# Kernel optimization log

Hardware: AMD Instinct MI355X
Metric: run time of the kernel (lower is better)

## Reference

```python
import jax, jax.numpy as jnp
import numpy as np

B, V_IN, V_OUT, C_IN, C_OUT, K, NNZ = 16, 1024, 4096, 128, 256, 18, 16384

def setup_inputs() -> dict:
    key = jax.random.key(0)
    ks = jax.random.split(key, 10)
    def lin(k, fan_in, fan_out):
        s = 1.0 / np.sqrt(fan_in)
        return jax.random.normal(k, (fan_in, fan_out), jnp.float32) * s
    return {
        "x": jax.random.normal(ks[0], (B, V_IN, C_IN), jnp.float32),
        "vals": jax.random.uniform(ks[1], (NNZ,), jnp.float32),
        "W1": lin(ks[2], 1 * C_IN, C_OUT),
        "b1": jnp.zeros((C_OUT,), jnp.float32),
        "Wd3": lin(ks[3], (K // 3) * C_IN, C_OUT // 4),
        "bd3": jnp.zeros((C_OUT // 4,), jnp.float32),
        "W2d3": lin(ks[4], (K // 3 * 2) * C_IN, C_OUT // 4),
        "b2d3": jnp.zeros((C_OUT // 4,), jnp.float32),
        "Wf": lin(ks[5], K * C_IN, C_OUT // 2),
        "bf": jnp.zeros((C_OUT // 2,), jnp.float32),
        "rows": jax.random.randint(ks[6], (NNZ,), 0, V_OUT, jnp.int32),
        "cols": jax.random.randint(ks[7], (NNZ,), 0, V_IN, jnp.int32),
        "spiral_idx": jax.random.randint(ks[8], (V_OUT, K), 0, V_OUT, jnp.int32),
    }

def _pool(x, rows, cols, vals, dim_size):
    # sparse upsample: gather cols, scale, scatter-add to rows
    gathered = x[:, cols, :] * vals[None, :, None]  # [B, nnz, C]
    return jnp.zeros((x.shape[0], dim_size, x.shape[2]), x.dtype).at[:, rows, :].add(gathered)

def _spiral_conv(feat, idx, W, b):
    # gather fixed spiral neighborhoods then shared linear layer
    Bz, V, C = feat.shape[0], idx.shape[0], feat.shape[2]
    g = feat[:, idx.reshape(-1), :].reshape(Bz, V, idx.shape[1] * C)  # [B, V, K*C]
    return g @ W + b

def reference(x, vals, W1, b1, Wd3, bd3, W2d3, b2d3, Wf, bf, rows, cols, spiral_idx):
    out = _pool(x, rows, cols, vals, V_OUT)  # [B, V_OUT, C_IN]
    k = spiral_idx.shape[1]
    short_cut = _spiral_conv(out, spiral_idx[:, :1], W1, b1)
    p_d3 = _spiral_conv(out, spiral_idx[:, : k // 3], Wd3, bd3)
    p_2d3 = _spiral_conv(out, spiral_idx[:, : k // 3 * 2], W2d3, b2d3)
    p = _spiral_conv(out, spiral_idx, Wf, bf)
    f = jnp.concatenate((p, p_2d3, p_d3), axis=2)  # [B, V_OUT, C_OUT]
    return jax.nn.relu(short_cut + f)
```

## Files before the change

### kernel.cpp

```cpp
#include <hip/hip_runtime.h>
#include <hip/hip_bf16.h>

#define B_SZ   16
#define V_IN   1024
#define V_OUT  4096
#define C_IN   128
#define C_OUT  256
#define K_NB   18
#define NNZ    16384
#define K_GEMM (K_NB * C_IN)
#define BK     64
#define NKT    (K_GEMM / BK)

typedef __attribute__((ext_vector_type(8))) short bf16x8;
typedef __attribute__((ext_vector_type(4))) float f32x4;

#define GLOAD16(src, dst) __builtin_amdgcn_global_load_lds( \
    (const __attribute__((address_space(1))) unsigned int*)(src), \
    (__attribute__((address_space(3))) unsigned int*)(dst), 16, 0, 0)

#define MFMA16(a_, b_, c_) __builtin_amdgcn_mfma_f32_16x16x32_bf16((a_), (b_), (c_), 0, 0, 0)

__global__ void hist_kernel(const int* __restrict__ rows, int* counts) {
    int n = blockIdx.x * blockDim.x + threadIdx.x;
    if (n < NNZ) atomicAdd(&counts[rows[n]], 1);
}

__global__ void scan_kernel(const int* __restrict__ counts, int* offsets, int* cursor) {
    __shared__ int wsum[16];
    int t = threadIdx.x;
    int lane = t & 63, wid = t >> 6;
    int base4 = t * 4;
    int c0 = counts[base4], c1 = counts[base4 + 1], c2 = counts[base4 + 2], c3 = counts[base4 + 3];
    int tot = c0 + c1 + c2 + c3;
    int v = tot;
#pragma unroll
    for (int d = 1; d < 64; d <<= 1) {
        int u = __shfl_up(v, d);
        if (lane >= d) v += u;
    }
    if (lane == 63) wsum[wid] = v;
    __syncthreads();
    int wbase = 0;
#pragma unroll
    for (int w = 0; w < 16; ++w) wbase += (w < wid) ? wsum[w] : 0;
    int incl = wbase + v;
    int excl = incl - tot;
    offsets[base4]     = excl;
    offsets[base4 + 1] = excl + c0;
    offsets[base4 + 2] = excl + c0 + c1;
    offsets[base4 + 3] = excl + c0 + c1 + c2;
    cursor[base4]     = excl;
    cursor[base4 + 1] = excl + c0;
    cursor[base4 + 2] = excl + c0 + c1;
    cursor[base4 + 3] = excl + c0 + c1 + c2;
    if (t == 1023) offsets[V_OUT] = incl;
}

__global__ void fill_kernel(const int* __restrict__ rows, int* cursor, int* perm) {
    int n = blockIdx.x * blockDim.x + threadIdx.x;
    if (n < NNZ) {
        int r = rows[n];
        int pos = atomicAdd(&cursor[r], 1);
        perm[pos] = n;
    }
}

__global__ __launch_bounds__(512) void pool_kernel(
    const float* __restrict__ x, const float* __restrict__ vals,
    const int* __restrict__ cols, const int* __restrict__ offsets,
    const int* __restrict__ perm, __hip_bfloat16* __restrict__ pool) {
    int r = blockIdx.x;
    int t = threadIdx.x;
    int b = t >> 5, c4 = t & 31;
    int j0 = offsets[r], j1 = offsets[r + 1];
    const float4* xb = (const float4*)x + (size_t)b * (V_IN * 32);
    float4 acc = {0.f, 0.f, 0.f, 0.f};
    for (int j = j0; j < j1; ++j) {
        int n = perm[j];
        float v = vals[n];
        float4 xv = xb[cols[n] * 32 + c4];
        acc.x += v * xv.x; acc.y += v * xv.y; acc.z += v * xv.z; acc.w += v * xv.w;
    }
    ushort4 o;
    o.x = __builtin_bit_cast(unsigned short, __float2bfloat16(acc.x));
    o.y = __builtin_bit_cast(unsigned short, __float2bfloat16(acc.y));
    o.z = __builtin_bit_cast(unsigned short, __float2bfloat16(acc.z));
    o.w = __builtin_bit_cast(unsigned short, __float2bfloat16(acc.w));
    ((ushort4*)pool)[((size_t)b * V_OUT + r) * 32 + c4] = o;
}

__global__ void wcomb_kernel(const float* __restrict__ W1, const float* __restrict__ Wd3,
                             const float* __restrict__ W2d3, const float* __restrict__ Wf,
                             const float* __restrict__ b1, const float* __restrict__ bd3,
                             const float* __restrict__ b2d3, const float* __restrict__ bf,
                             __hip_bfloat16* __restrict__ wTs, float* __restrict__ bias) {
    int idx = blockIdx.x * blockDim.x + threadIdx.x;
    if (idx >= NKT * 16384) {
        int c = idx - NKT * 16384;
        if (c < C_OUT) {
            float v = b1[c];
            if (c < 128)      v += bf[c];
            else if (c < 192) v += b2d3[c - 128];
            else              v += bd3[c - 192];
            bias[c] = v;
        }
        return;
    }
    int kt = idx >> 14;
    int c  = (idx >> 3) & 2047;
    int e  = idx & 7;
    int nrow  = c >> 3;
    int kslot = (c & 7) << 4;
    int kb = kslot ^ ((nrow & 7) << 4);
    int r  = kt * 64 + (kb >> 1) + e;
    int col = nrow;
    float v;
    if (col < 128)      v = Wf[r * 128 + col];
    else if (col < 192) v = (r < 1536) ? W2d3[r * 64 + (col - 128)] : 0.f;
    else                v = (r < 768)  ? Wd3[r * 64 + (col - 192)]  : 0.f;
    if (r < 128) v += W1[r * 256 + col];
    wTs[idx] = __float2bfloat16(v);
}

__global__ __launch_bounds__(512, 2) void gemm_kernel(
    const __hip_bfloat16* __restrict__ pool,
    const __hip_bfloat16* __restrict__ wTs,
    const float* __restrict__ bias,
    const int* __restrict__ spiral,
    float* __restrict__ out)
{
    __shared__ __align__(16) char smem[116736];
    int* spl = (int*)(smem + 98304);

    const int tid  = threadIdx.x;
    const int lane = tid & 63;
    const int wid  = tid >> 6;
    const int q    = wid & 3;
    const int wm   = (wid >> 2) << 7;

    const int bid = blockIdx.x;
    const int bm  = ((bid & 7) << 5) + (bid >> 3);
    const int b   = bm >> 4;
    const int v0  = (bm & 15) << 8;

    for (int i = tid; i < 256 * K_NB; i += 512) spl[i] = spiral[v0 * K_NB + i];
    asm volatile("s_waitcnt vmcnt(0) lgkmcnt(0)" ::: "memory");
    __builtin_amdgcn_s_barrier();

    const char* poolBytes = (const char*)(pool + (size_t)b * V_OUT * C_IN);
    const char* wTsBytes  = (const char*)wTs;
    const int sb = ((tid & 7) << 4) ^ (((tid >> 3) & 7) << 4);

    auto stageA = [&](int kt, int slot) {
        const int j   = kt >> 1;
        const int c0b = (kt & 1) << 7;
        char* dst = smem + (slot << 15);
#pragma unroll
        for (int ch = 0; ch < 4; ++ch) {
            int row  = (ch << 6) + (tid >> 3);
            int sidx = spl[row * K_NB + j];
            GLOAD16(poolBytes + ((size_t)sidx << 8) + (c0b + sb),
                    dst + (((ch << 9) + tid) << 4));
        }
    };

    const int l15   = lane & 15;
    const int swm   = (lane & 7) << 4;
    const int klane = (lane >> 4) << 4;
    const int kk0   = klane ^ swm;
    const int kk1   = (64 + klane) ^ swm;
    const int aBase = (wm + l15) << 7;
    const int bOff0 = (((2 * q)     << 4) + l15) << 7;
    const int bOff1 = (((2 * q + 1) << 4) + l15) << 7;
    const int bOff2 = (((8 + q)     << 4) + l15) << 7;
    const int bOff3 = (((12 + q)    << 4) + l15) << 7;

    f32x4 acc[8][4] = {};

    stageA(0, 0);
    stageA(1, 1);

    int sl = 0;
    for (int kt = 0; kt < NKT; ++kt) {
        if (kt + 1 < NKT) {
            asm volatile("s_waitcnt vmcnt(4)" ::: "memory");
        } else {
            asm volatile("s_waitcnt vmcnt(0)" ::: "memory");
        }
        __builtin_amdgcn_s_barrier();
        __builtin_amdgcn_sched_barrier(0);

        const char* As  = smem + (sl << 15);
        const char* wKt = wTsBytes + ((size_t)kt << 15);
        const bool doMid = kt < 24, doShort = kt < 12;

        bf16x8 b00, b01, b02, b03, b10, b11, b12, b13;
        b00 = *(const bf16x8*)(wKt + bOff0 + kk0);
        b01 = *(const bf16x8*)(wKt + bOff1 + kk0);
        if (doMid)   b02 = *(const bf16x8*)(wKt + bOff2 + kk0);
        if (doShort) b03 = *(const bf16x8*)(wKt + bOff3 + kk0);

        bf16x8 a[8];
#pragma unroll
        for (int mi = 0; mi < 8; ++mi)
            a[mi] = *(const bf16x8*)(As + aBase + (mi << 11) + kk0);

        b10 = *(const bf16x8*)(wKt + bOff0 + kk1);
        b11 = *(const bf16x8*)(wKt + bOff1 + kk1);
        if (doMid)   b12 = *(const bf16x8*)(wKt + bOff2 + kk1);
        if (doShort) b13 = *(const bf16x8*)(wKt + bOff3 + kk1);

        if (kt + 2 < NKT) {
            int st = sl + 2; if (st >= 3) st -= 3;
            stageA(kt + 2, st);
        }

        __builtin_amdgcn_s_setprio(1);
#pragma unroll
        for (int mi = 0; mi < 8; ++mi) {
            acc[mi][0] = MFMA16(a[mi], b00, acc[mi][0]);
            acc[mi][1] = MFMA16(a[mi], b01, acc[mi][1]);
        }
        if (doMid) {
#pragma unroll
            for (int mi = 0; mi < 8; ++mi) acc[mi][2] = MFMA16(a[mi], b02, acc[mi][2]);
        }
        if (doShort) {
#pragma unroll
            for (int mi = 0; mi < 8; ++mi) acc[mi][3] = MFMA16(a[mi], b03, acc[mi][3]);
        }
        __builtin_amdgcn_s_setprio(0);

#pragma unroll
        for (int mi = 0; mi < 8; ++mi)
            a[mi] = *(const bf16x8*)(As + aBase + (mi << 11) + kk1);

        __builtin_amdgcn_s_setprio(1);
#pragma unroll
        for (int mi = 0; mi < 8; ++mi) {
            acc[mi][0] = MFMA16(a[mi], b10, acc[mi][0]);
            acc[mi][1] = MFMA16(a[mi], b11, acc[mi][1]);
        }
        if (doMid) {
#pragma unroll
            for (int mi = 0; mi < 8; ++mi) acc[mi][2] = MFMA16(a[mi], b12, acc[mi][2]);
        }
        if (doShort) {
#pragma unroll
            for (int mi = 0; mi < 8; ++mi) acc[mi][3] = MFMA16(a[mi], b13, acc[mi][3]);
        }
        __builtin_amdgcn_s_setprio(0);

        sl += 1; if (sl >= 3) sl -= 3;
    }

    const int nt[4] = {2 * q, 2 * q + 1, 8 + q, 12 + q};
#pragma unroll
    for (int ni = 0; ni < 4; ++ni) {
        int col = (nt[ni] << 4) + l15;
        float bz = bias[col];
#pragma unroll
        for (int mi = 0; mi < 8; ++mi) {
            int row0 = v0 + wm + mi * 16 + ((lane >> 4) << 2);
#pragma unroll
            for (int r4 = 0; r4 < 4; ++r4) {
                float v = acc[mi][ni][r4] + bz;
                out[((size_t)(b * V_OUT + row0 + r4)) * C_OUT + col] = v > 0.f ? v : 0.f;
            }
        }
    }
}

extern "C" void kernel_launch(void* const* d_in, const int* in_sizes, int n_in,
                              void* d_out, int out_size, void* d_ws, size_t ws_size,
                              hipStream_t stream) {
    const float* x     = (const float*)d_in[0];
    const float* vals  = (const float*)d_in[1];
    const float* W1    = (const float*)d_in[2];
    const float* b1    = (const float*)d_in[3];
    const float* Wd3   = (const float*)d_in[4];
    const float* bd3   = (const float*)d_in[5];
    const float* W2d3  = (const float*)d_in[6];
    const float* b2d3  = (const float*)d_in[7];
    const float* Wf    = (const float*)d_in[8];
    const float* bf    = (const float*)d_in[9];
    const int*   rows  = (const int*)d_in[10];
    const int*   cols  = (const int*)d_in[11];
    const int*   spiral= (const int*)d_in[12];
    float* out = (float*)d_out;

    char* ws = (char*)d_ws;
    __hip_bfloat16* pool = (__hip_bfloat16*)ws;
    __hip_bfloat16* wTs  = (__hip_bfloat16*)(ws + 16777216);
    float* bias          = (float*)(ws + 16777216 + 1179648);
    int*   counts        = (int*)(ws + 16777216 + 1179648 + 1024);
    int*   offsets       = counts + V_OUT;
    int*   cursor        = offsets + V_OUT + 4;
    int*   perm          = cursor + V_OUT;

    hipMemsetAsync(counts, 0, V_OUT * sizeof(int), stream);
    hist_kernel<<<NNZ / 256, 256, 0, stream>>>(rows, counts);
    scan_kernel<<<1, 1024, 0, stream>>>(counts, offsets, cursor);
    fill_kernel<<<NNZ / 256, 256, 0, stream>>>(rows, cursor, perm);
    pool_kernel<<<V_OUT, 512, 0, stream>>>(x, vals, cols, offsets, perm, pool);
    wcomb_kernel<<<(NKT * 16384 + C_OUT + 255) / 256, 256, 0, stream>>>(
        W1, Wd3, W2d3, Wf, b1, bd3, b2d3, bf, wTs, bias);
    gemm_kernel<<<256, 512, 0, stream>>>(pool, wTs, bias, spiral, out);
}
```

Measured before the change: 115.0 us.

## Fuse CSR build into one kernel and halve GEMM tile for higher occupancy

Replaces the memset, histogram, scan and fill kernels with a single-block CSR kernel that uses shared-memory atomics, removing three launches and the global atomics. The GEMM block tile drops from 256 to 128 rows with 512 blocks, a smaller LDS footprint and 16-bit spiral indices, and launch bounds allow 4 blocks per CU. The MFMA/load schedule is also reordered so the second k-half loads are issued before staging the next tile. This costs less B-operand reuse per block (more weight-fragment reads per useful FLOP), and the single-block CSR pass serialises 16K atomics on one CU.

```diff
diff --git a/kernel.cpp b/kernel.cpp
--- a/kernel.cpp
+++ b/kernel.cpp
@@ -21,17 +21,21 @@
 
 #define MFMA16(a_, b_, c_) __builtin_amdgcn_mfma_f32_16x16x32_bf16((a_), (b_), (c_), 0, 0, 0)
 
-__global__ void hist_kernel(const int* __restrict__ rows, int* counts) {
-    int n = blockIdx.x * blockDim.x + threadIdx.x;
-    if (n < NNZ) atomicAdd(&counts[rows[n]], 1);
-}
-
-__global__ void scan_kernel(const int* __restrict__ counts, int* offsets, int* cursor) {
+__global__ __launch_bounds__(1024) void csr_kernel(const int* __restrict__ rows,
+                                                   int* __restrict__ offsets,
+                                                   int* __restrict__ perm) {
+    __shared__ int cnt[V_OUT];
     __shared__ int wsum[16];
-    int t = threadIdx.x;
-    int lane = t & 63, wid = t >> 6;
-    int base4 = t * 4;
-    int c0 = counts[base4], c1 = counts[base4 + 1], c2 = counts[base4 + 2], c3 = counts[base4 + 3];
+    const int t = threadIdx.x;
+    const int lane = t & 63, wid = t >> 6;
+#pragma unroll
+    for (int i = t; i < V_OUT; i += 1024) cnt[i] = 0;
+    __syncthreads();
+#pragma unroll
+    for (int n = t; n < NNZ; n += 1024) atomicAdd(&cnt[rows[n]], 1);
+    __syncthreads();
+    const int base4 = t * 4;
+    int c0 = cnt[base4], c1 = cnt[base4 + 1], c2 = cnt[base4 + 2], c3 = cnt[base4 + 3];
     int tot = c0 + c1 + c2 + c3;
     int v = tot;
 #pragma unroll
@@ -50,18 +54,16 @@
     offsets[base4 + 1] = excl + c0;
     offsets[base4 + 2] = excl + c0 + c1;
     offsets[base4 + 3] = excl + c0 + c1 + c2;
-    cursor[base4]     = excl;
-    cursor[base4 + 1] = excl + c0;
-    cursor[base4 + 2] = excl + c0 + c1;
-    cursor[base4 + 3] = excl + c0 + c1 + c2;
     if (t == 1023) offsets[V_OUT] = incl;
-}
-
-__global__ void fill_kernel(const int* __restrict__ rows, int* cursor, int* perm) {
-    int n = blockIdx.x * blockDim.x + threadIdx.x;
-    if (n < NNZ) {
-        int r = rows[n];
-        int pos = atomicAdd(&cursor[r], 1);
+    __syncthreads();
+    cnt[base4]     = excl;
+    cnt[base4 + 1] = excl + c0;
+    cnt[base4 + 2] = excl + c0 + c1;
+    cnt[base4 + 3] = excl + c0 + c1 + c2;
+    __syncthreads();
+#pragma unroll
+    for (int n = t; n < NNZ; n += 1024) {
+        int pos = atomicAdd(&cnt[rows[n]], 1);
         perm[pos] = n;
     }
 }
@@ -123,28 +125,29 @@
     wTs[idx] = __float2bfloat16(v);
 }
 
-__global__ __launch_bounds__(512, 2) void gemm_kernel(
+__global__ __launch_bounds__(512, 4) void gemm_kernel(
     const __hip_bfloat16* __restrict__ pool,
     const __hip_bfloat16* __restrict__ wTs,
     const float* __restrict__ bias,
     const int* __restrict__ spiral,
     float* __restrict__ out)
 {
-    __shared__ __align__(16) char smem[116736];
-    int* spl = (int*)(smem + 98304);
+    __shared__ __align__(16) char smem[53760];
+    unsigned short* spl = (unsigned short*)(smem + 49152);
 
     const int tid  = threadIdx.x;
     const int lane = tid & 63;
     const int wid  = tid >> 6;
     const int q    = wid & 3;
-    const int wm   = (wid >> 2) << 7;
+    const int wmL  = (wid >> 2) << 6;
 
     const int bid = blockIdx.x;
-    const int bm  = ((bid & 7) << 5) + (bid >> 3);
-    const int b   = bm >> 4;
-    const int v0  = (bm & 15) << 8;
-
-    for (int i = tid; i < 256 * K_NB; i += 512) spl[i] = spiral[v0 * K_NB + i];
+    const int bm  = ((bid & 7) << 6) + (bid >> 3);
+    const int b   = bm >> 5;
+    const int v0  = (bm & 31) << 7;
+
+    for (int i = tid; i < 128 * K_NB; i += 512)
+        spl[i] = (unsigned short)spiral[(v0 + i / K_NB) * K_NB + (i % K_NB)];
     asm volatile("s_waitcnt vmcnt(0) lgkmcnt(0)" ::: "memory");
     __builtin_amdgcn_s_barrier();
 
@@ -155,13 +158,12 @@
     auto stageA = [&](int kt, int slot) {
         const int j   = kt >> 1;
         const int c0b = (kt & 1) << 7;
-        char* dst = smem + (slot << 15);
-#pragma unroll
-        for (int ch = 0; ch < 4; ++ch) {
-            int row  = (ch << 6) + (tid >> 3);
-            int sidx = spl[row * K_NB + j];
-            GLOAD16(poolBytes + ((size_t)sidx << 8) + (c0b + sb),
-                    dst + (((ch << 9) + tid) << 4));
+        char* dst = smem + slot * 16384;
+#pragma unroll
+        for (int ch = 0; ch < 2; ++ch) {
+            int flat = (ch << 9) + tid;
+            int sidx = spl[(flat >> 3) * K_NB + j];
+            GLOAD16(poolBytes + ((size_t)sidx << 8) + (c0b + sb), dst + (flat << 4));
         }
     };
 
@@ -170,85 +172,78 @@
     const int klane = (lane >> 4) << 4;
     const int kk0   = klane ^ swm;
     const int kk1   = (64 + klane) ^ swm;
-    const int aBase = (wm + l15) << 7;
-    const int bOff0 = (((2 * q)     << 4) + l15) << 7;
-    const int bOff1 = (((2 * q + 1) << 4) + l15) << 7;
-    const int bOff2 = (((8 + q)     << 4) + l15) << 7;
-    const int bOff3 = (((12 + q)    << 4) + l15) << 7;
-
-    f32x4 acc[8][4] = {};
+    const int aBase = (wmL + l15) << 7;
+    const int bO0 = (((2 * q)     << 4) + l15) << 7;
+    const int bO1 = (((2 * q + 1) << 4) + l15) << 7;
+    const int bO2 = (((8 + q)     << 4) + l15) << 7;
+    const int bO3 = (((12 + q)    << 4) + l15) << 7;
+
+    f32x4 acc[4][4] = {};
 
     stageA(0, 0);
     stageA(1, 1);
 
     int sl = 0;
     for (int kt = 0; kt < NKT; ++kt) {
-        if (kt + 1 < NKT) {
-            asm volatile("s_waitcnt vmcnt(4)" ::: "memory");
-        } else {
-            asm volatile("s_waitcnt vmcnt(0)" ::: "memory");
-        }
+        if (kt + 1 < NKT) asm volatile("s_waitcnt vmcnt(2)" ::: "memory");
+        else              asm volatile("s_waitcnt vmcnt(0)" ::: "memory");
         __builtin_amdgcn_s_barrier();
         __builtin_amdgcn_sched_barrier(0);
 
-        const char* As  = smem + (sl << 15);
+        const char* As  = smem + sl * 16384;
         const char* wKt = wTsBytes + ((size_t)kt << 15);
         const bool doMid = kt < 24, doShort = kt < 12;
-
-        bf16x8 b00, b01, b02, b03, b10, b11, b12, b13;
-        b00 = *(const bf16x8*)(wKt + bOff0 + kk0);
-        b01 = *(const bf16x8*)(wKt + bOff1 + kk0);
-        if (doMid)   b02 = *(const bf16x8*)(wKt + bOff2 + kk0);
-        if (doShort) b03 = *(const bf16x8*)(wKt + bOff3 + kk0);
-
-        bf16x8 a[8];
-#pragma unroll
-        for (int mi = 0; mi < 8; ++mi)
+        bf16x8 a[4], b0, b1, b2, b3;
+
+        b0 = *(const bf16x8*)(wKt + bO0 + kk0);
+        b1 = *(const bf16x8*)(wKt + bO1 + kk0);
+        if (doMid)   b2 = *(const bf16x8*)(wKt + bO2 + kk0);
+        if (doShort) b3 = *(const bf16x8*)(wKt + bO3 + kk0);
+#pragma unroll
+        for (int mi = 0; mi < 4; ++mi)
             a[mi] = *(const bf16x8*)(As + aBase + (mi << 11) + kk0);
-
-        b10 = *(const bf16x8*)(wKt + bOff0 + kk1);
-        b11 = *(const bf16x8*)(wKt + bOff1 + kk1);
-        if (doMid)   b12 = *(const bf16x8*)(wKt + bOff2 + kk1);
-        if (doShort) b13 = *(const bf16x8*)(wKt + bOff3 + kk1);
-
+        __builtin_amdgcn_s_setprio(1);
+#pragma unroll
+        for (int mi = 0; mi < 4; ++mi) {
+            acc[mi][0] = MFMA16(a[mi], b0, acc[mi][0]);
+            acc[mi][1] = MFMA16(a[mi], b1, acc[mi][1]);
+        }
+        if (doMid) {
+#pragma unroll
+            for (int mi = 0; mi < 4; ++mi) acc[mi][2] = MFMA16(a[mi], b2, acc[mi][2]);
+        }
+        if (doShort) {
+#pragma unroll
+            for (int mi = 0; mi < 4; ++mi) acc[mi][3] = MFMA16(a[mi], b3, acc[mi][3]);
+        }
+        __builtin_amdgcn_s_setprio(0);
+
+        b0 = *(const bf16x8*)(wKt + bO0 + kk1);
+        b1 = *(const bf16x8*)(wKt + bO1 + kk1);
+        if (doMid)   b2 = *(const bf16x8*)(wKt + bO2 + kk1);
+        if (doShort) b3 = *(const bf16x8*)(wKt + bO3 + kk1);
+#pragma unroll
+        for (int mi = 0; mi < 4; ++mi)
+            a[mi] = *(const bf16x8*)(As + aBase + (mi << 11) + kk1);
+        __builtin_amdgcn_sched_barrier(0);
         if (kt + 2 < NKT) {
             int st = sl + 2; if (st >= 3) st -= 3;
             stageA(kt + 2, st);
         }
-
+        __builtin_amdgcn_sched_barrier(0);
         __builtin_amdgcn_s_setprio(1);
 #pragma unroll
-        for (int mi = 0; mi < 8; ++mi) {
-            acc[mi][0] = MFMA16(a[mi], b00, acc[mi][0]);
-            acc[mi][1] = MFMA16(a[mi], b01, acc[mi][1]);
+        for (int mi = 0; mi < 4; ++mi) {
+            acc[mi][0] = MFMA16(a[mi], b0, acc[mi][0]);
+            acc[mi][1] = MFMA16(a[mi], b1, acc[mi][1]);
         }
         if (doMid) {
 #pragma unroll
-            for (int mi = 0; mi < 8; ++mi) acc[mi][2] = MFMA16(a[mi], b02, acc[mi][2]);
+            for (int mi = 0; mi < 4; ++mi) acc[mi][2] = MFMA16(a[mi], b2, acc[mi][2]);
         }
         if (doShort) {
 #pragma unroll
-            for (int mi = 0; mi < 8; ++mi) acc[mi][3] = MFMA16(a[mi], b03, acc[mi][3]);
-        }
-        __builtin_amdgcn_s_setprio(0);
-
-#pragma unroll
-        for (int mi = 0; mi < 8; ++mi)
-            a[mi] = *(const bf16x8*)(As + aBase + (mi << 11) + kk1);
-
-        __builtin_amdgcn_s_setprio(1);
-#pragma unroll
-        for (int mi = 0; mi < 8; ++mi) {
-            acc[mi][0] = MFMA16(a[mi], b10, acc[mi][0]);
-            acc[mi][1] = MFMA16(a[mi], b11, acc[mi][1]);
-        }
-        if (doMid) {
-#pragma unroll
-            for (int mi = 0; mi < 8; ++mi) acc[mi][2] = MFMA16(a[mi], b12, acc[mi][2]);
-        }
-        if (doShort) {
-#pragma unroll
-            for (int mi = 0; mi < 8; ++mi) acc[mi][3] = MFMA16(a[mi], b13, acc[mi][3]);
+            for (int mi = 0; mi < 4; ++mi) acc[mi][3] = MFMA16(a[mi], b3, acc[mi][3]);
         }
         __builtin_amdgcn_s_setprio(0);
 
@@ -261,8 +256,8 @@
         int col = (nt[ni] << 4) + l15;
         float bz = bias[col];
 #pragma unroll
-        for (int mi = 0; mi < 8; ++mi) {
-            int row0 = v0 + wm + mi * 16 + ((lane >> 4) << 2);
+        for (int mi = 0; mi < 4; ++mi) {
+            int row0 = v0 + wmL + mi * 16 + ((lane >> 4) << 2);
 #pragma unroll
             for (int r4 = 0; r4 < 4; ++r4) {
                 float v = acc[mi][ni][r4] + bz;
@@ -294,17 +289,12 @@
     __hip_bfloat16* pool = (__hip_bfloat16*)ws;
     __hip_bfloat16* wTs  = (__hip_bfloat16*)(ws + 16777216);
     float* bias          = (float*)(ws + 16777216 + 1179648);
-    int*   counts        = (int*)(ws + 16777216 + 1179648 + 1024);
-    int*   offsets       = counts + V_OUT;
-    int*   cursor        = offsets + V_OUT + 4;
-    int*   perm          = cursor + V_OUT;
-
-    hipMemsetAsync(counts, 0, V_OUT * sizeof(int), stream);
-    hist_kernel<<<NNZ / 256, 256, 0, stream>>>(rows, counts);
-    scan_kernel<<<1, 1024, 0, stream>>>(counts, offsets, cursor);
-    fill_kernel<<<NNZ / 256, 256, 0, stream>>>(rows, cursor, perm);
+    int*   offsets       = (int*)(ws + 16777216 + 1179648 + 1024);
+    int*   perm          = offsets + V_OUT + 4;
+
+    csr_kernel<<<1, 1024, 0, stream>>>(rows, offsets, perm);
     pool_kernel<<<V_OUT, 512, 0, stream>>>(x, vals, cols, offsets, perm, pool);
     wcomb_kernel<<<(NKT * 16384 + C_OUT + 255) / 256, 256, 0, stream>>>(
         W1, Wd3, W2d3, Wf, b1, bd3, b2d3, bf, wTs, bias);
-    gemm_kernel<<<256, 512, 0, stream>>>(pool, wTs, bias, spiral, out);
-}
+    gemm_kernel<<<512, 512, 0, stream>>>(pool, wTs, bias, spiral, out);
+}
```

Result: slower. 121.1 us (+5.3%).
